# Kernel optimization log

Measured on AMD Instinct MI355X. Metric: run time of the kernel, lower is better.

## Reference

```python
import jax, jax.numpy as jnp
import numpy as np

B, S, C, V, LAT, NL = 256, 512, 256, 32, 256, 7
DILS = [1, 2, 4, 8, 16, 32, 64]
EPS = 1e-5


def setup_inputs() -> dict:
    key = jax.random.key(0)
    ks = jax.random.split(key, 24)
    s = 0.05
    inp = {
        "x": jax.random.randint(ks[0], (B, S), 0, V, dtype=jnp.int64 if jax.config.read("jax_enable_x64") else jnp.int32),
        "z": jax.random.normal(ks[1], (B, LAT), dtype=jnp.float32),
        "emb": jax.random.normal(ks[2], (V, C), dtype=jnp.float32) * s,
        "latent_W": jax.random.normal(ks[3], (LAT, C), dtype=jnp.float32) * s,
        "latent_b": jnp.zeros((C,), jnp.float32),
        "ln1_g": jnp.ones((NL, C), jnp.float32),
        "ln1_b": jnp.zeros((NL, C), jnp.float32),
        "w1": jax.random.normal(ks[4], (NL, C, C), jnp.float32) * s,
        "b1": jnp.zeros((NL, C), jnp.float32),
        "ln2_g": jnp.ones((NL, C), jnp.float32),
        "ln2_b": jnp.zeros((NL, C), jnp.float32),
        "wd": jax.random.normal(ks[5], (NL, 2, C, C), jnp.float32) * s,  # tap 0 = x[t-d], tap 1 = x[t]
        "bd": jnp.zeros((NL, C), jnp.float32),
        "ln3_g": jnp.ones((NL, C), jnp.float32),
        "ln3_b": jnp.zeros((NL, C), jnp.float32),
        "we": jax.random.normal(ks[6], (NL, C, C), jnp.float32) * s,
        "be": jnp.zeros((NL, C), jnp.float32),
        "wg": jax.random.normal(ks[7], (NL, C, C), jnp.float32) * s,
        "bg": jnp.zeros((NL, C), jnp.float32),
        "out_W": jax.random.normal(ks[8], (C, V), jnp.float32) * s,
        "out_b": jnp.zeros((V,), jnp.float32),
    }
    return inp


def _ln(h, g, b):
    mu = h.mean(-1, keepdims=True)
    var = jnp.mean((h - mu) ** 2, axis=-1, keepdims=True)
    return (h - mu) * jax.lax.rsqrt(var + EPS) * g + b


def _lrelu(h):
    return jnp.where(h >= 0, h, 0.01 * h)


def reference(x, z, emb, latent_W, latent_b, ln1_g, ln1_b, w1, b1,
              ln2_g, ln2_b, wd, bd, ln3_g, ln3_b, we, be, wg, bg,
              out_W, out_b):
    # channel-last layout [B, S, C] throughout (fuses away the torch transposes)
    h = emb[x] + (z @ latent_W + latent_b)[:, None, :]
    for i, d in enumerate(DILS):
        x_inp = h
        t = _lrelu(_ln(x_inp, ln1_g[i], ln1_b[i]))
        t = t @ w1[i] + b1[i]
        t = _lrelu(_ln(t, ln2_g[i], ln2_b[i]))
        # causal dilated conv, kernel=2: out[t] = W0*x[t-d] + W1*x[t]
        t_shift = jnp.pad(t, ((0, 0), (d, 0), (0, 0)))[:, :t.shape[1], :]
        t = t_shift @ wd[i, 0] + t @ wd[i, 1] + bd[i]
        t = _lrelu(_ln(t, ln3_g[i], ln3_b[i]))
        gated = (t @ we[i] + be[i]) * jax.nn.sigmoid(t @ wg[i] + bg[i])
        h = gated + x_inp
    logits = h @ out_W + out_b                      # [B, S, V]
    lp = jax.nn.log_softmax(logits, axis=-1)
    # gather log-prob of next token: lp[:, :-1, :] at x[:, 1:]
    return jnp.take_along_axis(lp[:, :-1, :], x[:, 1:, None], axis=2)[..., 0]
```

## Files before the change

kernel.cpp:

```cpp
#include <hip/hip_runtime.h>

typedef unsigned short u16;
typedef unsigned int   u32;
typedef __attribute__((ext_vector_type(8))) short short8;
typedef __attribute__((ext_vector_type(4))) float f32x4;

struct __align__(8) u16x4 { u16 x, y, z, w; };

#define NL 7
#define M_DIM 131072

__device__ __forceinline__ float b2f(u16 u) {
  union { float f; u32 i; } c; c.i = ((u32)u) << 16; return c.f;
}
__device__ __forceinline__ u16 f2b(float f) {
  union { float f; u32 i; } c; c.f = f;
  u32 r = c.i + 0x7FFFu + ((c.i >> 16) & 1u);
  return (u16)(r >> 16);
}
__device__ __forceinline__ void gload16(const void* g, void* l) {
  __builtin_amdgcn_global_load_lds((const __attribute__((address_space(1))) void*)g,
                                   (__attribute__((address_space(3))) void*)l, 16, 0, 0);
}


__global__ __launch_bounds__(256) void conv_w1_k(const float* __restrict__ w1, u16* __restrict__ wT) {
  int idx = blockIdx.x * 256 + threadIdx.x;
  int i = idx >> 16, rem = idx & 65535;
  int n = rem >> 8, k = rem & 255;
  wT[idx] = f2b(w1[(i << 16) + (k << 8) + n]);
}

__global__ __launch_bounds__(256) void conv_wd_k(const float* __restrict__ wd, u16* __restrict__ wT) {
  int idx = blockIdx.x * 256 + threadIdx.x;
  int i = idx / 131072, rem = idx & 131071;
  int n = rem >> 9, k2 = rem & 511;
  int tap = k2 >> 8, k = k2 & 255;
  wT[idx] = f2b(wd[(((i * 2 + tap) << 8) + k) * 256 + n]);
}

__global__ __launch_bounds__(256) void conv_weg_k(const float* __restrict__ we, const float* __restrict__ wg,
                                                  u16* __restrict__ wT) {
  int idx = blockIdx.x * 256 + threadIdx.x;
  int i = idx / 131072, rem = idx & 131071;
  int src = rem >> 16, n = (rem >> 8) & 255, k = rem & 255;
  const float* W = src ? wg : we;
  wT[idx] = f2b(W[((i << 8) + k) * 256 + n]);
}

__global__ __launch_bounds__(256) void conv_wo_k(const float* __restrict__ outW, u16* __restrict__ wTo) {
  int idx = blockIdx.x * 256 + threadIdx.x;
  int v = idx >> 8, k = idx & 255;
  wTo[idx] = f2b(outW[k * 32 + v]);
}


__global__ __launch_bounds__(256) void zlat_k(const float* __restrict__ z, const float* __restrict__ W,
                                              const float* __restrict__ bias, float* __restrict__ zlat) {
  int b = blockIdx.x, c = threadIdx.x;
  float acc = bias[c];
  for (int l = 0; l < 256; ++l) acc += z[b * 256 + l] * W[l * 256 + c];
  zlat[b * 256 + c] = acc;
}


__global__ __launch_bounds__(256) void embed_k(const int* __restrict__ x, const float* __restrict__ emb,
                                               const float* __restrict__ zlat, u16* __restrict__ h) {
  int wave = threadIdx.x >> 6, lane = threadIdx.x & 63;
  int r = blockIdx.x * 4 + wave;
  int c = lane * 4;
  int tok = x[r];
  int bi = r >> 9;
  float4 ev = *(const float4*)&emb[tok * 256 + c];
  float4 zv = *(const float4*)&zlat[bi * 256 + c];
  u16x4 hb;
  hb.x = f2b(ev.x + zv.x); hb.y = f2b(ev.y + zv.y);
  hb.z = f2b(ev.z + zv.z); hb.w = f2b(ev.w + zv.w);
  *(u16x4*)&h[(long)r * 256 + c] = hb;
}


__global__ __launch_bounds__(256, 2) void gemm1_k(
    const u16* __restrict__ h, const u16* __restrict__ WT,
    const float* __restrict__ ln1g, const float* __restrict__ ln1b,
    const float* __restrict__ bias,
    const float* __restrict__ ln2g, const float* __restrict__ ln2b,
    u16* __restrict__ V)
{
  __shared__ __align__(16) u16 lA[64 * 264];
  __shared__ __align__(16) u16 lB[256 * 32];
  __shared__ float pS[64][4], pQ[64][4];
  __shared__ float muA[64], rsA[64];
  const int tid = threadIdx.x;
  const int lane = tid & 63;
  const int wv = tid >> 6;
  const int wc = wv * 64;
  const int m0 = blockIdx.x * 64;
  const int rA = tid >> 2;
  const int cSw = ((((tid & 3) - ((tid >> 3) & 3)) & 3)) * 8;
  const int lr = lane & 15;
  const int quad = lane >> 4;
  const int lq = quad * 8;
  const int sw = ((quad + ((lr >> 1) & 3)) & 3) * 8;

  {
    const int half = lane >> 5, l5 = lane & 31;
    float4 ga = *(const float4*)&ln1g[l5 * 8];
    float4 gb = *(const float4*)&ln1g[l5 * 8 + 4];
    float4 ba = *(const float4*)&ln1b[l5 * 8];
    float4 bb = *(const float4*)&ln1b[l5 * 8 + 4];
    #pragma unroll 4
    for (int it = 0; it < 8; ++it) {
      int row = wv * 16 + it * 2 + half;
      uint4 hv = *(const uint4*)(h + (long)(m0 + row) * 256 + l5 * 8);
      float v0 = b2f((u16)(hv.x & 0xffff)), v1 = b2f((u16)(hv.x >> 16));
      float v2 = b2f((u16)(hv.y & 0xffff)), v3 = b2f((u16)(hv.y >> 16));
      float v4 = b2f((u16)(hv.z & 0xffff)), v5 = b2f((u16)(hv.z >> 16));
      float v6 = b2f((u16)(hv.w & 0xffff)), v7 = b2f((u16)(hv.w >> 16));
      float s = v0 + v1 + v2 + v3 + v4 + v5 + v6 + v7;
      float q = v0*v0 + v1*v1 + v2*v2 + v3*v3 + v4*v4 + v5*v5 + v6*v6 + v7*v7;
      #pragma unroll
      for (int o = 1; o < 32; o <<= 1) { s += __shfl_xor(s, o); q += __shfl_xor(q, o); }
      float mu = s * 0.00390625f;
      float var = q * 0.00390625f - mu * mu;
      float rs = rsqrtf(var + 1e-5f);
      float y0 = (v0 - mu) * rs * ga.x + ba.x; y0 = y0 >= 0.f ? y0 : 0.01f * y0;
      float y1 = (v1 - mu) * rs * ga.y + ba.y; y1 = y1 >= 0.f ? y1 : 0.01f * y1;
      float y2 = (v2 - mu) * rs * ga.z + ba.z; y2 = y2 >= 0.f ? y2 : 0.01f * y2;
      float y3 = (v3 - mu) * rs * ga.w + ba.w; y3 = y3 >= 0.f ? y3 : 0.01f * y3;
      float y4 = (v4 - mu) * rs * gb.x + bb.x; y4 = y4 >= 0.f ? y4 : 0.01f * y4;
      float y5 = (v5 - mu) * rs * gb.y + bb.y; y5 = y5 >= 0.f ? y5 : 0.01f * y5;
      float y6 = (v6 - mu) * rs * gb.z + bb.z; y6 = y6 >= 0.f ? y6 : 0.01f * y6;
      float y7 = (v7 - mu) * rs * gb.w + bb.w; y7 = y7 >= 0.f ? y7 : 0.01f * y7;
      uint4 ov;
      ov.x = (u32)f2b(y0) | ((u32)f2b(y1) << 16);
      ov.y = (u32)f2b(y2) | ((u32)f2b(y3) << 16);
      ov.z = (u32)f2b(y4) | ((u32)f2b(y5) << 16);
      ov.w = (u32)f2b(y6) | ((u32)f2b(y7) << 16);
      *(uint4*)&lA[row * 264 + l5 * 8] = ov;
    }
  }

  f32x4 acc[4][4];
  #pragma unroll
  for (int i = 0; i < 4; ++i)
    #pragma unroll
    for (int j = 0; j < 4; ++j) {
      acc[i][j][0] = 0.f; acc[i][j][1] = 0.f; acc[i][j][2] = 0.f; acc[i][j][3] = 0.f;
    }

  for (int kt = 0; kt < 8; ++kt) {
    const int kk = kt * 32;
    const long bofs = (long)rA * 256 + kk + cSw;
    #pragma unroll
    for (int j = 0; j < 4; ++j)
      gload16(WT + bofs + (long)(64 * j) * 256, &lB[tid * 8 + j * 2048]);
    __syncthreads();

    short8 af[4], bfr[4];
    #pragma unroll
    for (int mt = 0; mt < 4; ++mt)
      af[mt] = *(const short8*)&lA[(mt * 16 + lr) * 264 + kk + lq];
    #pragma unroll
    for (int nt = 0; nt < 4; ++nt)
      bfr[nt] = *(const short8*)&lB[(wc + nt * 16 + lr) * 32 + sw];
    #pragma unroll
    for (int mt = 0; mt < 4; ++mt)
      #pragma unroll
      for (int nt = 0; nt < 4; ++nt)
        acc[mt][nt] = __builtin_amdgcn_mfma_f32_16x16x32_bf16(af[mt], bfr[nt], acc[mt][nt], 0, 0, 0);
    __syncthreads();
  }

  float biasv[4], gv[4], bv[4];
  #pragma unroll
  for (int nt = 0; nt < 4; ++nt) {
    int n = wc + nt * 16 + lr;
    biasv[nt] = bias[n]; gv[nt] = ln2g[n]; bv[nt] = ln2b[n];
  }
  #pragma unroll
  for (int mt = 0; mt < 4; ++mt)
    #pragma unroll
    for (int r = 0; r < 4; ++r) {
      float s = 0.f, q = 0.f;
      #pragma unroll
      for (int nt = 0; nt < 4; ++nt) {
        float v = acc[mt][nt][r] + biasv[nt];
        acc[mt][nt][r] = v;
        s += v; q += v * v;
      }
      #pragma unroll
      for (int o = 1; o < 16; o <<= 1) { s += __shfl_xor(s, o); q += __shfl_xor(q, o); }
      if (lr == 0) { pS[mt * 16 + quad * 4 + r][wv] = s; pQ[mt * 16 + quad * 4 + r][wv] = q; }
    }
  __syncthreads();
  if (tid < 64) {
    float S = pS[tid][0] + pS[tid][1] + pS[tid][2] + pS[tid][3];
    float Q = pQ[tid][0] + pQ[tid][1] + pQ[tid][2] + pQ[tid][3];
    float mu = S * 0.00390625f;
    float var = Q * 0.00390625f - mu * mu;
    muA[tid] = mu; rsA[tid] = rsqrtf(var + 1e-5f);
  }
  __syncthreads();
  #pragma unroll
  for (int mt = 0; mt < 4; ++mt)
    #pragma unroll
    for (int r = 0; r < 4; ++r) {
      int row = mt * 16 + quad * 4 + r;
      float mu = muA[row], rs = rsA[row];
      #pragma unroll
      for (int nt = 0; nt < 4; ++nt) {
        float y = (acc[mt][nt][r] - mu) * rs * gv[nt] + bv[nt];
        y = y >= 0.f ? y : 0.01f * y;
        V[(long)(m0 + row) * 256 + wc + nt * 16 + lr] = f2b(y);
      }
    }
}


__global__ __launch_bounds__(256, 2) void conv_gate_k(
    const u16* __restrict__ A,
    const u16* __restrict__ WTd,
    int dil,
    const float* __restrict__ bd3, const float* __restrict__ g3, const float* __restrict__ bb3,
    const u16* __restrict__ WTe, const u16* __restrict__ WTg,
    const float* __restrict__ bev_, const float* __restrict__ bgv_,
    u16* __restrict__ h)
{
  __shared__ __align__(16) u16 pT[64 * 264];
  __shared__ __align__(16) u16 stg[16384];
  __shared__ float pS[64][4], pQ[64][4];
  __shared__ float muA[64], rsA[64];

  const int tid = threadIdx.x;
  const int lane = tid & 63;
  const int wv = tid >> 6;
  const int wc = wv * 64;
  const int m0 = blockIdx.x * 64;
  const int rA = tid >> 2;
  const int cSw = ((((tid & 3) - ((tid >> 3) & 3)) & 3)) * 8;
  const int lr = lane & 15;
  const int quad = lane >> 4;
  const int lq = quad * 8;
  const int sw = ((quad + ((lr >> 1) & 3)) & 3) * 8;
  const int mm = m0 + rA;
  const int s1 = mm & 511;
  const bool fixBlk = (m0 & 511) == 0;

  f32x4 acc[4][4];
  #pragma unroll
  for (int i = 0; i < 4; ++i)
    #pragma unroll
    for (int j = 0; j < 4; ++j) {
      acc[i][j][0] = 0.f; acc[i][j][1] = 0.f; acc[i][j][2] = 0.f; acc[i][j][3] = 0.f;
    }

#define STAGE_P1(KT) do {                                                        \
    const int kt_ = (KT);                                                        \
    const int kk_ = (kt_ & 7) * 32;                                              \
    const int r_ = (kt_ < 8 && s1 >= dil) ? (mm - dil) : mm;                     \
    gload16(A + (long)r_ * 256 + kk_ + cSw, &stg[tid * 8]);                      \
    const u16* bSrc_ = WTd + kt_ * 32 + cSw;                                     \
    gload16(bSrc_ + (long)rA * 512,         &stg[2048 + tid * 8]);               \
    gload16(bSrc_ + (long)(rA + 64) * 512,  &stg[2048 + tid * 8 + 2048]);        \
    gload16(bSrc_ + (long)(rA + 128) * 512, &stg[2048 + tid * 8 + 4096]);        \
    gload16(bSrc_ + (long)(rA + 192) * 512, &stg[2048 + tid * 8 + 6144]);        \
  } while (0)

  STAGE_P1(0);
  __syncthreads();

  for (int kt = 0; kt < 16; ++kt) {
    if (fixBlk && kt < 8) {
      if (rA < dil) { uint4 zz; zz.x = 0; zz.y = 0; zz.z = 0; zz.w = 0; *(uint4*)&stg[tid * 8] = zz; }
      __syncthreads();
    }
    short8 af[4], bfr[4];
    #pragma unroll
    for (int mt = 0; mt < 4; ++mt)
      af[mt] = *(const short8*)&stg[(mt * 16 + lr) * 32 + sw];
    #pragma unroll
    for (int nt = 0; nt < 4; ++nt)
      bfr[nt] = *(const short8*)&stg[2048 + (wc + nt * 16 + lr) * 32 + sw];
    __syncthreads();
    if (kt < 15) STAGE_P1(kt + 1);
    #pragma unroll
    for (int mt = 0; mt < 4; ++mt)
      #pragma unroll
      for (int nt = 0; nt < 4; ++nt)
        acc[mt][nt] = __builtin_amdgcn_mfma_f32_16x16x32_bf16(af[mt], bfr[nt], acc[mt][nt], 0, 0, 0);
    __syncthreads();
  }
#undef STAGE_P1

#define STAGE_P2(KT) do {                                                        \
    const long bofs_ = (long)rA * 256 + (KT) * 32 + cSw;                         \
    gload16(WTe + bofs_,              &stg[tid * 8]);                            \
    gload16(WTe + bofs_ + 64L * 256,  &stg[tid * 8 + 2048]);                     \
    gload16(WTe + bofs_ + 128L * 256, &stg[tid * 8 + 4096]);                     \
    gload16(WTe + bofs_ + 192L * 256, &stg[tid * 8 + 6144]);                     \
    gload16(WTg + bofs_,              &stg[8192 + tid * 8]);                     \
    gload16(WTg + bofs_ + 64L * 256,  &stg[8192 + tid * 8 + 2048]);              \
    gload16(WTg + bofs_ + 128L * 256, &stg[8192 + tid * 8 + 4096]);              \
    gload16(WTg + bofs_ + 192L * 256, &stg[8192 + tid * 8 + 6144]);              \
  } while (0)

  STAGE_P2(0);

  float b3v[4], g3v[4], o3v[4];
  #pragma unroll
  for (int nt = 0; nt < 4; ++nt) {
    int n = wc + nt * 16 + lr;
    b3v[nt] = bd3[n]; g3v[nt] = g3[n]; o3v[nt] = bb3[n];
  }
  #pragma unroll
  for (int mt = 0; mt < 4; ++mt)
    #pragma unroll
    for (int r = 0; r < 4; ++r) {
      float s = 0.f, q = 0.f;
      #pragma unroll
      for (int nt = 0; nt < 4; ++nt) {
        float v = acc[mt][nt][r] + b3v[nt];
        acc[mt][nt][r] = v;
        s += v; q += v * v;
      }
      #pragma unroll
      for (int o = 1; o < 16; o <<= 1) { s += __shfl_xor(s, o); q += __shfl_xor(q, o); }
      if (lr == 0) { pS[mt * 16 + quad * 4 + r][wv] = s; pQ[mt * 16 + quad * 4 + r][wv] = q; }
    }
  __syncthreads();
  if (tid < 64) {
    float S = pS[tid][0] + pS[tid][1] + pS[tid][2] + pS[tid][3];
    float Q = pQ[tid][0] + pQ[tid][1] + pQ[tid][2] + pQ[tid][3];
    float mu = S * 0.00390625f;
    float var = Q * 0.00390625f - mu * mu;
    muA[tid] = mu; rsA[tid] = rsqrtf(var + 1e-5f);
  }
  __syncthreads();
  #pragma unroll
  for (int mt = 0; mt < 4; ++mt)
    #pragma unroll
    for (int r = 0; r < 4; ++r) {
      int row = mt * 16 + quad * 4 + r;
      float mu = muA[row], rs = rsA[row];
      #pragma unroll
      for (int nt = 0; nt < 4; ++nt) {
        float y = (acc[mt][nt][r] - mu) * rs * g3v[nt] + o3v[nt];
        y = y >= 0.f ? y : 0.01f * y;
        pT[row * 264 + wc + nt * 16 + lr] = f2b(y);
      }
    }
  __syncthreads();

  f32x4 accE[4][4], accG[4][4];
  #pragma unroll
  for (int i = 0; i < 4; ++i)
    #pragma unroll
    for (int j = 0; j < 4; ++j) {
      accE[i][j][0] = 0.f; accE[i][j][1] = 0.f; accE[i][j][2] = 0.f; accE[i][j][3] = 0.f;
      accG[i][j][0] = 0.f; accG[i][j][1] = 0.f; accG[i][j][2] = 0.f; accG[i][j][3] = 0.f;
    }

  for (int kt = 0; kt < 8; ++kt) {
    const int kk = kt * 32;
    short8 paf[4], bfe[4], bfg[4];
    #pragma unroll
    for (int mt = 0; mt < 4; ++mt)
      paf[mt] = *(const short8*)&pT[(mt * 16 + lr) * 264 + kk + lq];
    #pragma unroll
    for (int nt = 0; nt < 4; ++nt) {
      bfe[nt] = *(const short8*)&stg[(wc + nt * 16 + lr) * 32 + sw];
      bfg[nt] = *(const short8*)&stg[8192 + (wc + nt * 16 + lr) * 32 + sw];
    }
    __syncthreads();
    if (kt < 7) STAGE_P2(kt + 1);
    #pragma unroll
    for (int mt = 0; mt < 4; ++mt)
      #pragma unroll
      for (int nt = 0; nt < 4; ++nt) {
        accE[mt][nt] = __builtin_amdgcn_mfma_f32_16x16x32_bf16(paf[mt], bfe[nt], accE[mt][nt], 0, 0, 0);
        accG[mt][nt] = __builtin_amdgcn_mfma_f32_16x16x32_bf16(paf[mt], bfg[nt], accG[mt][nt], 0, 0, 0);
      }
    __syncthreads();
  }
#undef STAGE_P2

  float bev[4], bgv[4];
  #pragma unroll
  for (int nt = 0; nt < 4; ++nt) {
    int n = wc + nt * 16 + lr;
    bev[nt] = bev_[n]; bgv[nt] = bgv_[n];
  }
  #pragma unroll
  for (int mt = 0; mt < 4; ++mt)
    #pragma unroll
    for (int r = 0; r < 4; ++r) {
      int row = mt * 16 + quad * 4 + r;
      long off = (long)(m0 + row) * 256;
      #pragma unroll
      for (int nt = 0; nt < 4; ++nt) {
        int n = wc + nt * 16 + lr;
        float e = accE[mt][nt][r] + bev[nt];
        float gg = accG[mt][nt][r] + bgv[nt];
        float hn = e * (1.f / (1.f + expf(-gg))) + b2f(h[off + n]);
        h[off + n] = f2b(hn);
      }
    }
}


__global__ __launch_bounds__(256) void final_k(const u16* __restrict__ h, const u16* __restrict__ WTo,
                                               const float* __restrict__ outb, const int* __restrict__ x,
                                               float* __restrict__ out) {
  __shared__ u16 lW[32 * 264];
  const int tid = threadIdx.x;
  const int lane = tid & 63;
  const int wv = tid >> 6;
  const int mBase = blockIdx.x * 256 + wv * 64;

  #pragma unroll
  for (int j = 0; j < 4; ++j) {
    int chunk = tid + 256 * j;
    int v = chunk >> 5, k8 = chunk & 31;
    uint4 w4 = *(const uint4*)(WTo + v * 256 + k8 * 8);
    *(uint4*)&lW[v * 264 + k8 * 8] = w4;
  }
  __syncthreads();

  const int lq = (lane >> 4) * 8;
  const int lr = lane & 15;
  const int quad = lane >> 4;

  f32x4 acc[4][2];
  #pragma unroll
  for (int mt = 0; mt < 4; ++mt) {
    acc[mt][0][0] = 0.f; acc[mt][0][1] = 0.f; acc[mt][0][2] = 0.f; acc[mt][0][3] = 0.f;
    acc[mt][1][0] = 0.f; acc[mt][1][1] = 0.f; acc[mt][1][2] = 0.f; acc[mt][1][3] = 0.f;
  }

  for (int kt = 0; kt < 8; ++kt) {
    short8 bf0 = *(const short8*)&lW[lr * 264 + kt * 32 + lq];
    short8 bf1 = *(const short8*)&lW[(16 + lr) * 264 + kt * 32 + lq];
    #pragma unroll
    for (int mt = 0; mt < 4; ++mt) {
      short8 af = *(const short8*)(h + (long)(mBase + mt * 16 + lr) * 256 + kt * 32 + lq);
      acc[mt][0] = __builtin_amdgcn_mfma_f32_16x16x32_bf16(af, bf0, acc[mt][0], 0, 0, 0);
      acc[mt][1] = __builtin_amdgcn_mfma_f32_16x16x32_bf16(af, bf1, acc[mt][1], 0, 0, 0);
    }
  }

  float ob0 = outb[lr], ob1 = outb[16 + lr];
  #pragma unroll
  for (int mt = 0; mt < 4; ++mt)
    #pragma unroll
    for (int r = 0; r < 4; ++r) {
      int row = mBase + mt * 16 + quad * 4 + r;
      float lo = acc[mt][0][r] + ob0;
      float hi = acc[mt][1][r] + ob1;
      float mx = fmaxf(lo, hi);
      #pragma unroll
      for (int o = 1; o < 16; o <<= 1) mx = fmaxf(mx, __shfl_xor(mx, o));
      float se = expf(lo - mx) + expf(hi - mx);
      #pragma unroll
      for (int o = 1; o < 16; o <<= 1) se += __shfl_xor(se, o);
      int s = row & 511;
      int xa = (s == 511) ? row : (row + 1);
      int tok = x[xa];
      float lg = (tok < 16) ? lo : hi;
      float lp = lg - mx - logf(se);
      if (s != 511 && lr == (tok & 15))
        out[(row >> 9) * 511 + s] = lp;
    }
}


extern "C" void kernel_launch(void* const* d_in, const int* in_sizes, int n_in,
                              void* d_out, int out_size, void* d_ws, size_t ws_size,
                              hipStream_t stream) {
  const int*   x    = (const int*)d_in[0];
  const float* z    = (const float*)d_in[1];
  const float* emb  = (const float*)d_in[2];
  const float* latW = (const float*)d_in[3];
  const float* latb = (const float*)d_in[4];
  const float* ln1g = (const float*)d_in[5];
  const float* ln1b = (const float*)d_in[6];
  const float* w1   = (const float*)d_in[7];
  const float* b1   = (const float*)d_in[8];
  const float* ln2g = (const float*)d_in[9];
  const float* ln2b = (const float*)d_in[10];
  const float* wd   = (const float*)d_in[11];
  const float* bd   = (const float*)d_in[12];
  const float* ln3g = (const float*)d_in[13];
  const float* ln3b = (const float*)d_in[14];
  const float* we   = (const float*)d_in[15];
  const float* be   = (const float*)d_in[16];
  const float* wg   = (const float*)d_in[17];
  const float* bg   = (const float*)d_in[18];
  const float* outW = (const float*)d_in[19];
  const float* outb = (const float*)d_in[20];

  char* ws = (char*)d_ws;
  u16*   h    = (u16*)(ws + 0);
  u16*   bufA = (u16*)(ws + 67108864);
  float* zlat = (float*)(ws + 201326592);
  u16*   wT1  = (u16*)(ws + 201588736);
  u16*   wTd  = (u16*)(ws + 202506240);
  u16*   wTeg = (u16*)(ws + 204341248);
  u16*   wTo  = (u16*)(ws + 206176256);

  conv_w1_k <<<1792, 256, 0, stream>>>(w1, wT1);
  conv_wd_k <<<3584, 256, 0, stream>>>(wd, wTd);
  conv_weg_k<<<3584, 256, 0, stream>>>(we, wg, wTeg);
  conv_wo_k <<<32, 256, 0, stream>>>(outW, wTo);
  zlat_k    <<<256, 256, 0, stream>>>(z, latW, latb, zlat);
  embed_k   <<<M_DIM / 4, 256, 0, stream>>>(x, emb, zlat, h);

  for (int i = 0; i < NL; ++i) {
    int d = 1 << i;
    gemm1_k<<<M_DIM / 64, 256, 0, stream>>>(
        h, wT1 + i * 65536, ln1g + i * 256, ln1b + i * 256, b1 + i * 256,
        ln2g + i * 256, ln2b + i * 256, bufA);
    conv_gate_k<<<M_DIM / 64, 256, 0, stream>>>(
        bufA, wTd + i * 131072, d,
        bd + i * 256, ln3g + i * 256, ln3b + i * 256,
        wTeg + i * 131072, wTeg + i * 131072 + 65536,
        be + i * 256, bg + i * 256, h);
  }

  final_k<<<M_DIM / 256, 256, 0, stream>>>(h, wTo, outb, x, (float*)d_out);
}
```

Measured before the change: 1.467 ms.

## Double-buffer conv_gate staging with explicit waitcnt and split E/G GEMM loops

```diff
diff --git a/kernel.cpp b/kernel.cpp
--- a/kernel.cpp
+++ b/kernel.cpp
@@ -9,6 +9,10 @@
 
 #define NL 7
 #define M_DIM 131072
+
+#define VMW(N) asm volatile("s_waitcnt vmcnt(" #N ")" ::: "memory")
+#define LGW()  asm volatile("s_waitcnt lgkmcnt(0)" ::: "memory")
+#define BAR()  __builtin_amdgcn_s_barrier()
 
 __device__ __forceinline__ float b2f(u16 u) {
   union { float f; u32 i; } c; c.i = ((u32)u) << 16; return c.f;
@@ -228,7 +232,7 @@
     u16* __restrict__ h)
 {
   __shared__ __align__(16) u16 pT[64 * 264];
-  __shared__ __align__(16) u16 stg[16384];
+  __shared__ __align__(16) u16 stg[20480];
   __shared__ float pS[64][4], pQ[64][4];
   __shared__ float muA[64], rsA[64];
 
@@ -246,6 +250,25 @@
   const int mm = m0 + rA;
   const int s1 = mm & 511;
   const bool fixBlk = (m0 & 511) == 0;
+  const short8 zero8 = {0, 0, 0, 0, 0, 0, 0, 0};
+
+  auto STAGE1 = [&](int kt, int bb) {
+    const int kkk = (kt & 7) * 32;
+    const int rr = (kt < 8 && s1 >= dil) ? (mm - dil) : mm;
+    gload16(A + (long)rr * 256 + kkk + cSw, &stg[bb + tid * 8]);
+    const u16* bS = WTd + kt * 32 + cSw;
+    gload16(bS + (long)rA * 512,          &stg[bb + 2048 + tid * 8]);
+    gload16(bS + (long)(rA + 64) * 512,   &stg[bb + 4096 + tid * 8]);
+    gload16(bS + (long)(rA + 128) * 512,  &stg[bb + 6144 + tid * 8]);
+    gload16(bS + (long)(rA + 192) * 512,  &stg[bb + 8192 + tid * 8]);
+  };
+  auto STAGE_W = [&](const u16* __restrict__ W, int kt, int bb) {
+    const long bofs = (long)rA * 256 + kt * 32 + cSw;
+    gload16(W + bofs,              &stg[bb + tid * 8]);
+    gload16(W + bofs + 64L * 256,  &stg[bb + 2048 + tid * 8]);
+    gload16(W + bofs + 128L * 256, &stg[bb + 4096 + tid * 8]);
+    gload16(W + bofs + 192L * 256, &stg[bb + 6144 + tid * 8]);
+  };
 
   f32x4 acc[4][4];
   #pragma unroll
@@ -255,57 +278,40 @@
       acc[i][j][0] = 0.f; acc[i][j][1] = 0.f; acc[i][j][2] = 0.f; acc[i][j][3] = 0.f;
     }
 
-#define STAGE_P1(KT) do {                                                        \
-    const int kt_ = (KT);                                                        \
-    const int kk_ = (kt_ & 7) * 32;                                              \
-    const int r_ = (kt_ < 8 && s1 >= dil) ? (mm - dil) : mm;                     \
-    gload16(A + (long)r_ * 256 + kk_ + cSw, &stg[tid * 8]);                      \
-    const u16* bSrc_ = WTd + kt_ * 32 + cSw;                                     \
-    gload16(bSrc_ + (long)rA * 512,         &stg[2048 + tid * 8]);               \
-    gload16(bSrc_ + (long)(rA + 64) * 512,  &stg[2048 + tid * 8 + 2048]);        \
-    gload16(bSrc_ + (long)(rA + 128) * 512, &stg[2048 + tid * 8 + 4096]);        \
-    gload16(bSrc_ + (long)(rA + 192) * 512, &stg[2048 + tid * 8 + 6144]);        \
-  } while (0)
-
-  STAGE_P1(0);
-  __syncthreads();
-
-  for (int kt = 0; kt < 16; ++kt) {
-    if (fixBlk && kt < 8) {
-      if (rA < dil) { uint4 zz; zz.x = 0; zz.y = 0; zz.z = 0; zz.w = 0; *(uint4*)&stg[tid * 8] = zz; }
-      __syncthreads();
-    }
+  STAGE1(0, 0);
+  STAGE1(1, 10240);
+  VMW(5);
+  BAR();
+
+  #pragma unroll
+  for (int r = 0; r < 16; ++r) {
+    const int bb = (r & 1) * 10240;
     short8 af[4], bfr[4];
     #pragma unroll
     for (int mt = 0; mt < 4; ++mt)
-      af[mt] = *(const short8*)&stg[(mt * 16 + lr) * 32 + sw];
+      af[mt] = *(const short8*)&stg[bb + (mt * 16 + lr) * 32 + sw];
     #pragma unroll
     for (int nt = 0; nt < 4; ++nt)
-      bfr[nt] = *(const short8*)&stg[2048 + (wc + nt * 16 + lr) * 32 + sw];
-    __syncthreads();
-    if (kt < 15) STAGE_P1(kt + 1);
+      bfr[nt] = *(const short8*)&stg[bb + 2048 + (wc + nt * 16 + lr) * 32 + sw];
+    LGW();
+    BAR();
+    if (r <= 13)      STAGE1(r + 2, bb);
+    else if (r == 14) STAGE_W(WTe, 0, 0);
+    else              STAGE_W(WTe, 1, 8192);
+    if (fixBlk && r < 8) {
+      #pragma unroll
+      for (int mt = 0; mt < 4; ++mt)
+        if (mt * 16 + lr < dil) af[mt] = zero8;
+    }
     #pragma unroll
     for (int mt = 0; mt < 4; ++mt)
       #pragma unroll
       for (int nt = 0; nt < 4; ++nt)
         acc[mt][nt] = __builtin_amdgcn_mfma_f32_16x16x32_bf16(af[mt], bfr[nt], acc[mt][nt], 0, 0, 0);
-    __syncthreads();
-  }
-#undef STAGE_P1
-
-#define STAGE_P2(KT) do {                                                        \
-    const long bofs_ = (long)rA * 256 + (KT) * 32 + cSw;                         \
-    gload16(WTe + bofs_,              &stg[tid * 8]);                            \
-    gload16(WTe + bofs_ + 64L * 256,  &stg[tid * 8 + 2048]);                     \
-    gload16(WTe + bofs_ + 128L * 256, &stg[tid * 8 + 4096]);                     \
-    gload16(WTe + bofs_ + 192L * 256, &stg[tid * 8 + 6144]);                     \
-    gload16(WTg + bofs_,              &stg[8192 + tid * 8]);                     \
-    gload16(WTg + bofs_ + 64L * 256,  &stg[8192 + tid * 8 + 2048]);              \
-    gload16(WTg + bofs_ + 128L * 256, &stg[8192 + tid * 8 + 4096]);              \
-    gload16(WTg + bofs_ + 192L * 256, &stg[8192 + tid * 8 + 6144]);              \
-  } while (0)
-
-  STAGE_P2(0);
+    if (r <= 13)      VMW(5);
+    else if (r == 14) VMW(4);
+    BAR();
+  }
 
   float b3v[4], g3v[4], o3v[4];
   #pragma unroll
@@ -328,7 +334,7 @@
       for (int o = 1; o < 16; o <<= 1) { s += __shfl_xor(s, o); q += __shfl_xor(q, o); }
       if (lr == 0) { pS[mt * 16 + quad * 4 + r][wv] = s; pQ[mt * 16 + quad * 4 + r][wv] = q; }
     }
-  __syncthreads();
+  LGW(); BAR();
   if (tid < 64) {
     float S = pS[tid][0] + pS[tid][1] + pS[tid][2] + pS[tid][3];
     float Q = pQ[tid][0] + pQ[tid][1] + pQ[tid][2] + pQ[tid][3];
@@ -336,7 +342,7 @@
     float var = Q * 0.00390625f - mu * mu;
     muA[tid] = mu; rsA[tid] = rsqrtf(var + 1e-5f);
   }
-  __syncthreads();
+  LGW(); BAR();
   #pragma unroll
   for (int mt = 0; mt < 4; ++mt)
     #pragma unroll
@@ -350,7 +356,7 @@
         pT[row * 264 + wc + nt * 16 + lr] = f2b(y);
       }
     }
-  __syncthreads();
+  LGW(); VMW(4); BAR();
 
   f32x4 accE[4][4], accG[4][4];
   #pragma unroll
@@ -361,29 +367,50 @@
       accG[i][j][0] = 0.f; accG[i][j][1] = 0.f; accG[i][j][2] = 0.f; accG[i][j][3] = 0.f;
     }
 
-  for (int kt = 0; kt < 8; ++kt) {
-    const int kk = kt * 32;
-    short8 paf[4], bfe[4], bfg[4];
-    #pragma unroll
-    for (int mt = 0; mt < 4; ++mt)
-      paf[mt] = *(const short8*)&pT[(mt * 16 + lr) * 264 + kk + lq];
-    #pragma unroll
-    for (int nt = 0; nt < 4; ++nt) {
-      bfe[nt] = *(const short8*)&stg[(wc + nt * 16 + lr) * 32 + sw];
-      bfg[nt] = *(const short8*)&stg[8192 + (wc + nt * 16 + lr) * 32 + sw];
-    }
-    __syncthreads();
-    if (kt < 7) STAGE_P2(kt + 1);
-    #pragma unroll
-    for (int mt = 0; mt < 4; ++mt)
-      #pragma unroll
-      for (int nt = 0; nt < 4; ++nt) {
+  #pragma unroll
+  for (int r = 0; r < 8; ++r) {
+    const int bb = (r & 1) * 8192;
+    short8 paf[4], bfe[4];
+    #pragma unroll
+    for (int mt = 0; mt < 4; ++mt)
+      paf[mt] = *(const short8*)&pT[(mt * 16 + lr) * 264 + r * 32 + lq];
+    #pragma unroll
+    for (int nt = 0; nt < 4; ++nt)
+      bfe[nt] = *(const short8*)&stg[bb + (wc + nt * 16 + lr) * 32 + sw];
+    LGW(); BAR();
+    if (r <= 5)      STAGE_W(WTe, r + 2, bb);
+    else if (r == 6) STAGE_W(WTg, 0, 0);
+    else             STAGE_W(WTg, 1, 8192);
+    #pragma unroll
+    for (int mt = 0; mt < 4; ++mt)
+      #pragma unroll
+      for (int nt = 0; nt < 4; ++nt)
         accE[mt][nt] = __builtin_amdgcn_mfma_f32_16x16x32_bf16(paf[mt], bfe[nt], accE[mt][nt], 0, 0, 0);
+    VMW(4);
+    BAR();
+  }
+
+  #pragma unroll
+  for (int r = 0; r < 8; ++r) {
+    const int bb = (r & 1) * 8192;
+    short8 paf[4], bfg[4];
+    #pragma unroll
+    for (int mt = 0; mt < 4; ++mt)
+      paf[mt] = *(const short8*)&pT[(mt * 16 + lr) * 264 + r * 32 + lq];
+    #pragma unroll
+    for (int nt = 0; nt < 4; ++nt)
+      bfg[nt] = *(const short8*)&stg[bb + (wc + nt * 16 + lr) * 32 + sw];
+    LGW(); BAR();
+    if (r <= 5) STAGE_W(WTg, r + 2, bb);
+    #pragma unroll
+    for (int mt = 0; mt < 4; ++mt)
+      #pragma unroll
+      for (int nt = 0; nt < 4; ++nt)
         accG[mt][nt] = __builtin_amdgcn_mfma_f32_16x16x32_bf16(paf[mt], bfg[nt], accG[mt][nt], 0, 0, 0);
-      }
-    __syncthreads();
-  }
-#undef STAGE_P2
+    if (r <= 5)      VMW(4);
+    else if (r == 6) VMW(0);
+    BAR();
+  }
 
   float bev[4], bgv[4];
   #pragma unroll
```

Result: faster. 1.436 ms (-2.1%).

## Load GEMM operands directly from global memory into registers, dropping LDS staging

Applied to the files above, without the earlier changes.

```diff
diff --git a/kernel.cpp b/kernel.cpp
--- a/kernel.cpp
+++ b/kernel.cpp
@@ -17,10 +17,6 @@
   union { float f; u32 i; } c; c.f = f;
   u32 r = c.i + 0x7FFFu + ((c.i >> 16) & 1u);
   return (u16)(r >> 16);
-}
-__device__ __forceinline__ void gload16(const void* g, void* l) {
-  __builtin_amdgcn_global_load_lds((const __attribute__((address_space(1))) void*)g,
-                                   (__attribute__((address_space(3))) void*)l, 16, 0, 0);
 }
 
 
@@ -80,7 +76,7 @@
 }
 
 
-__global__ __launch_bounds__(256, 2) void gemm1_k(
+__global__ __launch_bounds__(256, 4) void gemm1_k(
     const u16* __restrict__ h, const u16* __restrict__ WT,
     const float* __restrict__ ln1g, const float* __restrict__ ln1b,
     const float* __restrict__ bias,
@@ -88,7 +84,6 @@
     u16* __restrict__ V)
 {
   __shared__ __align__(16) u16 lA[64 * 264];
-  __shared__ __align__(16) u16 lB[256 * 32];
   __shared__ float pS[64][4], pQ[64][4];
   __shared__ float muA[64], rsA[64];
   const int tid = threadIdx.x;
@@ -96,12 +91,9 @@
   const int wv = tid >> 6;
   const int wc = wv * 64;
   const int m0 = blockIdx.x * 64;
-  const int rA = tid >> 2;
-  const int cSw = ((((tid & 3) - ((tid >> 3) & 3)) & 3)) * 8;
   const int lr = lane & 15;
   const int quad = lane >> 4;
   const int lq = quad * 8;
-  const int sw = ((quad + ((lr >> 1) & 3)) & 3) * 8;
 
   {
     const int half = lane >> 5, l5 = lane & 31;
@@ -149,27 +141,27 @@
       acc[i][j][0] = 0.f; acc[i][j][1] = 0.f; acc[i][j][2] = 0.f; acc[i][j][3] = 0.f;
     }
 
+  const u16* bp[4];
+  #pragma unroll
+  for (int nt = 0; nt < 4; ++nt) bp[nt] = WT + (long)(wc + nt * 16 + lr) * 256 + lq;
+
+  __syncthreads();
+
+  #pragma unroll
   for (int kt = 0; kt < 8; ++kt) {
     const int kk = kt * 32;
-    const long bofs = (long)rA * 256 + kk + cSw;
-    #pragma unroll
-    for (int j = 0; j < 4; ++j)
-      gload16(WT + bofs + (long)(64 * j) * 256, &lB[tid * 8 + j * 2048]);
-    __syncthreads();
-
     short8 af[4], bfr[4];
+    #pragma unroll
+    for (int nt = 0; nt < 4; ++nt)
+      bfr[nt] = *(const short8*)(bp[nt] + kk);
     #pragma unroll
     for (int mt = 0; mt < 4; ++mt)
       af[mt] = *(const short8*)&lA[(mt * 16 + lr) * 264 + kk + lq];
     #pragma unroll
-    for (int nt = 0; nt < 4; ++nt)
-      bfr[nt] = *(const short8*)&lB[(wc + nt * 16 + lr) * 32 + sw];
-    #pragma unroll
     for (int mt = 0; mt < 4; ++mt)
       #pragma unroll
       for (int nt = 0; nt < 4; ++nt)
         acc[mt][nt] = __builtin_amdgcn_mfma_f32_16x16x32_bf16(af[mt], bfr[nt], acc[mt][nt], 0, 0, 0);
-    __syncthreads();
   }
 
   float biasv[4], gv[4], bv[4];
@@ -228,7 +220,6 @@
     u16* __restrict__ h)
 {
   __shared__ __align__(16) u16 pT[64 * 264];
-  __shared__ __align__(16) u16 stg[16384];
   __shared__ float pS[64][4], pQ[64][4];
   __shared__ float muA[64], rsA[64];
 
@@ -237,15 +228,10 @@
   const int wv = tid >> 6;
   const int wc = wv * 64;
   const int m0 = blockIdx.x * 64;
-  const int rA = tid >> 2;
-  const int cSw = ((((tid & 3) - ((tid >> 3) & 3)) & 3)) * 8;
   const int lr = lane & 15;
   const int quad = lane >> 4;
   const int lq = quad * 8;
-  const int sw = ((quad + ((lr >> 1) & 3)) & 3) * 8;
-  const int mm = m0 + rA;
-  const int s1 = mm & 511;
-  const bool fixBlk = (m0 & 511) == 0;
+  const short8 zero8 = {0, 0, 0, 0, 0, 0, 0, 0};
 
   f32x4 acc[4][4];
   #pragma unroll
@@ -255,57 +241,43 @@
       acc[i][j][0] = 0.f; acc[i][j][1] = 0.f; acc[i][j][2] = 0.f; acc[i][j][3] = 0.f;
     }
 
-#define STAGE_P1(KT) do {                                                        \
-    const int kt_ = (KT);                                                        \
-    const int kk_ = (kt_ & 7) * 32;                                              \
-    const int r_ = (kt_ < 8 && s1 >= dil) ? (mm - dil) : mm;                     \
-    gload16(A + (long)r_ * 256 + kk_ + cSw, &stg[tid * 8]);                      \
-    const u16* bSrc_ = WTd + kt_ * 32 + cSw;                                     \
-    gload16(bSrc_ + (long)rA * 512,         &stg[2048 + tid * 8]);               \
-    gload16(bSrc_ + (long)(rA + 64) * 512,  &stg[2048 + tid * 8 + 2048]);        \
-    gload16(bSrc_ + (long)(rA + 128) * 512, &stg[2048 + tid * 8 + 4096]);        \
-    gload16(bSrc_ + (long)(rA + 192) * 512, &stg[2048 + tid * 8 + 6144]);        \
-  } while (0)
-
-  STAGE_P1(0);
-  __syncthreads();
-
+  const u16* a0p[4];
+  const u16* a1p[4];
+  bool zz[4];
+  #pragma unroll
+  for (int mt = 0; mt < 4; ++mt) {
+    int row = m0 + mt * 16 + lr;
+    int ss = row & 511;
+    zz[mt] = ss < dil;
+    a1p[mt] = A + (long)row * 256 + lq;
+    a0p[mt] = A + (long)(zz[mt] ? row : row - dil) * 256 + lq;
+  }
+  const u16* bdp[4];
+  #pragma unroll
+  for (int nt = 0; nt < 4; ++nt) bdp[nt] = WTd + (long)(wc + nt * 16 + lr) * 512 + lq;
+
+  #pragma unroll
   for (int kt = 0; kt < 16; ++kt) {
-    if (fixBlk && kt < 8) {
-      if (rA < dil) { uint4 zz; zz.x = 0; zz.y = 0; zz.z = 0; zz.w = 0; *(uint4*)&stg[tid * 8] = zz; }
-      __syncthreads();
-    }
+    const int kk = (kt & 7) * 32;
     short8 af[4], bfr[4];
     #pragma unroll
-    for (int mt = 0; mt < 4; ++mt)
-      af[mt] = *(const short8*)&stg[(mt * 16 + lr) * 32 + sw];
-    #pragma unroll
     for (int nt = 0; nt < 4; ++nt)
-      bfr[nt] = *(const short8*)&stg[2048 + (wc + nt * 16 + lr) * 32 + sw];
-    __syncthreads();
-    if (kt < 15) STAGE_P1(kt + 1);
+      bfr[nt] = *(const short8*)(bdp[nt] + kt * 32);
+    #pragma unroll
+    for (int mt = 0; mt < 4; ++mt) {
+      if (kt < 8) {
+        af[mt] = *(const short8*)(a0p[mt] + kk);
+        if (zz[mt]) af[mt] = zero8;
+      } else {
+        af[mt] = *(const short8*)(a1p[mt] + kk);
+      }
+    }
     #pragma unroll
     for (int mt = 0; mt < 4; ++mt)
       #pragma unroll
       for (int nt = 0; nt < 4; ++nt)
         acc[mt][nt] = __builtin_amdgcn_mfma_f32_16x16x32_bf16(af[mt], bfr[nt], acc[mt][nt], 0, 0, 0);
-    __syncthreads();
-  }
-#undef STAGE_P1
-
-#define STAGE_P2(KT) do {                                                        \
-    const long bofs_ = (long)rA * 256 + (KT) * 32 + cSw;                         \
-    gload16(WTe + bofs_,              &stg[tid * 8]);                            \
-    gload16(WTe + bofs_ + 64L * 256,  &stg[tid * 8 + 2048]);                     \
-    gload16(WTe + bofs_ + 128L * 256, &stg[tid * 8 + 4096]);                     \
-    gload16(WTe + bofs_ + 192L * 256, &stg[tid * 8 + 6144]);                     \
-    gload16(WTg + bofs_,              &stg[8192 + tid * 8]);                     \
-    gload16(WTg + bofs_ + 64L * 256,  &stg[8192 + tid * 8 + 2048]);              \
-    gload16(WTg + bofs_ + 128L * 256, &stg[8192 + tid * 8 + 4096]);              \
-    gload16(WTg + bofs_ + 192L * 256, &stg[8192 + tid * 8 + 6144]);              \
-  } while (0)
-
-  STAGE_P2(0);
+  }
 
   float b3v[4], g3v[4], o3v[4];
   #pragma unroll
@@ -361,19 +333,25 @@
       accG[i][j][0] = 0.f; accG[i][j][1] = 0.f; accG[i][j][2] = 0.f; accG[i][j][3] = 0.f;
     }
 
+  const u16* bep[4]; const u16* bgp[4];
+  #pragma unroll
+  for (int nt = 0; nt < 4; ++nt) {
+    long ro = (long)(wc + nt * 16 + lr) * 256 + lq;
+    bep[nt] = WTe + ro; bgp[nt] = WTg + ro;
+  }
+
+  #pragma unroll
   for (int kt = 0; kt < 8; ++kt) {
     const int kk = kt * 32;
     short8 paf[4], bfe[4], bfg[4];
     #pragma unroll
+    for (int nt = 0; nt < 4; ++nt) {
+      bfe[nt] = *(const short8*)(bep[nt] + kk);
+      bfg[nt] = *(const short8*)(bgp[nt] + kk);
+    }
+    #pragma unroll
     for (int mt = 0; mt < 4; ++mt)
       paf[mt] = *(const short8*)&pT[(mt * 16 + lr) * 264 + kk + lq];
-    #pragma unroll
-    for (int nt = 0; nt < 4; ++nt) {
-      bfe[nt] = *(const short8*)&stg[(wc + nt * 16 + lr) * 32 + sw];
-      bfg[nt] = *(const short8*)&stg[8192 + (wc + nt * 16 + lr) * 32 + sw];
-    }
-    __syncthreads();
-    if (kt < 7) STAGE_P2(kt + 1);
     #pragma unroll
     for (int mt = 0; mt < 4; ++mt)
       #pragma unroll
@@ -381,9 +359,7 @@
         accE[mt][nt] = __builtin_amdgcn_mfma_f32_16x16x32_bf16(paf[mt], bfe[nt], accE[mt][nt], 0, 0, 0);
         accG[mt][nt] = __builtin_amdgcn_mfma_f32_16x16x32_bf16(paf[mt], bfg[nt], accG[mt][nt], 0, 0, 0);
       }
-    __syncthreads();
-  }
-#undef STAGE_P2
+  }
 
   float bev[4], bgv[4];
   #pragma unroll
```

New measurement: 1.982 ms. 1.35x slower.

## Shrink LDS footprint to fit three blocks per CU in fused layer kernels

Applied to the files above, without the earlier changes.

```diff
diff --git a/kernel.cpp b/kernel.cpp
--- a/kernel.cpp
+++ b/kernel.cpp
@@ -21,6 +21,9 @@
 __device__ __forceinline__ void gload16(const void* g, void* l) {
   __builtin_amdgcn_global_load_lds((const __attribute__((address_space(1))) void*)g,
                                    (__attribute__((address_space(3))) void*)l, 16, 0, 0);
+}
+__device__ __forceinline__ int xIdx(int row, int chunk) {
+  return row * 256 + (((chunk) ^ (row & 7)) << 3);
 }
 
 
@@ -80,17 +83,19 @@
 }
 
 
-__global__ __launch_bounds__(256, 2) void gemm1_k(
+__global__ __launch_bounds__(256, 3) void gemm1_k(
     const u16* __restrict__ h, const u16* __restrict__ WT,
     const float* __restrict__ ln1g, const float* __restrict__ ln1b,
     const float* __restrict__ bias,
     const float* __restrict__ ln2g, const float* __restrict__ ln2b,
     u16* __restrict__ V)
 {
-  __shared__ __align__(16) u16 lA[64 * 264];
+  __shared__ __align__(16) u16 lA[64 * 256];
   __shared__ __align__(16) u16 lB[256 * 32];
-  __shared__ float pS[64][4], pQ[64][4];
-  __shared__ float muA[64], rsA[64];
+  float* pS  = (float*)lB;
+  float* pQ  = (float*)(lB + 512);
+  float* muA = (float*)(lB + 1024);
+  float* rsA = (float*)(lB + 1152);
   const int tid = threadIdx.x;
   const int lane = tid & 63;
   const int wv = tid >> 6;
@@ -100,7 +105,6 @@
   const int cSw = ((((tid & 3) - ((tid >> 3) & 3)) & 3)) * 8;
   const int lr = lane & 15;
   const int quad = lane >> 4;
-  const int lq = quad * 8;
   const int sw = ((quad + ((lr >> 1) & 3)) & 3) * 8;
 
   {
@@ -137,7 +141,7 @@
       ov.y = (u32)f2b(y2) | ((u32)f2b(y3) << 16);
       ov.z = (u32)f2b(y4) | ((u32)f2b(y5) << 16);
       ov.w = (u32)f2b(y6) | ((u32)f2b(y7) << 16);
-      *(uint4*)&lA[row * 264 + l5 * 8] = ov;
+      *(uint4*)&lA[xIdx(row, l5)] = ov;
     }
   }
 
@@ -150,8 +154,7 @@
     }
 
   for (int kt = 0; kt < 8; ++kt) {
-    const int kk = kt * 32;
-    const long bofs = (long)rA * 256 + kk + cSw;
+    const long bofs = (long)rA * 256 + kt * 32 + cSw;
     #pragma unroll
     for (int j = 0; j < 4; ++j)
       gload16(WT + bofs + (long)(64 * j) * 256, &lB[tid * 8 + j * 2048]);
@@ -160,7 +163,7 @@
     short8 af[4], bfr[4];
     #pragma unroll
     for (int mt = 0; mt < 4; ++mt)
-      af[mt] = *(const short8*)&lA[(mt * 16 + lr) * 264 + kk + lq];
+      af[mt] = *(const short8*)&lA[xIdx(mt * 16 + lr, 4 * kt + quad)];
     #pragma unroll
     for (int nt = 0; nt < 4; ++nt)
       bfr[nt] = *(const short8*)&lB[(wc + nt * 16 + lr) * 32 + sw];
@@ -191,12 +194,12 @@
       }
       #pragma unroll
       for (int o = 1; o < 16; o <<= 1) { s += __shfl_xor(s, o); q += __shfl_xor(q, o); }
-      if (lr == 0) { pS[mt * 16 + quad * 4 + r][wv] = s; pQ[mt * 16 + quad * 4 + r][wv] = q; }
+      if (lr == 0) { pS[(mt * 16 + quad * 4 + r) * 4 + wv] = s; pQ[(mt * 16 + quad * 4 + r) * 4 + wv] = q; }
     }
   __syncthreads();
   if (tid < 64) {
-    float S = pS[tid][0] + pS[tid][1] + pS[tid][2] + pS[tid][3];
-    float Q = pQ[tid][0] + pQ[tid][1] + pQ[tid][2] + pQ[tid][3];
+    float S = pS[tid * 4 + 0] + pS[tid * 4 + 1] + pS[tid * 4 + 2] + pS[tid * 4 + 3];
+    float Q = pQ[tid * 4 + 0] + pQ[tid * 4 + 1] + pQ[tid * 4 + 2] + pQ[tid * 4 + 3];
     float mu = S * 0.00390625f;
     float var = Q * 0.00390625f - mu * mu;
     muA[tid] = mu; rsA[tid] = rsqrtf(var + 1e-5f);
@@ -218,7 +221,7 @@
 }
 
 
-__global__ __launch_bounds__(256, 2) void conv_gate_k(
+__global__ __launch_bounds__(256, 3) void conv_gate_k(
     const u16* __restrict__ A,
     const u16* __restrict__ WTd,
     int dil,
@@ -227,10 +230,13 @@
     const float* __restrict__ bev_, const float* __restrict__ bgv_,
     u16* __restrict__ h)
 {
-  __shared__ __align__(16) u16 pT[64 * 264];
-  __shared__ __align__(16) u16 stg[16384];
-  __shared__ float pS[64][4], pQ[64][4];
-  __shared__ float muA[64], rsA[64];
+  __shared__ __align__(16) u16 pT[64 * 256];
+  __shared__ __align__(16) u16 stg[10240];
+  float* pS  = (float*)stg;
+  float* pQ  = (float*)(stg + 512);
+  float* muA = (float*)(stg + 1024);
+  float* rsA = (float*)(stg + 1152);
+  u16* stgW = stg + 2048;
 
   const int tid = threadIdx.x;
   const int lane = tid & 63;
@@ -241,11 +247,15 @@
   const int cSw = ((((tid & 3) - ((tid >> 3) & 3)) & 3)) * 8;
   const int lr = lane & 15;
   const int quad = lane >> 4;
-  const int lq = quad * 8;
   const int sw = ((quad + ((lr >> 1) & 3)) & 3) * 8;
   const int mm = m0 + rA;
   const int s1 = mm & 511;
-  const bool fixBlk = (m0 & 511) == 0;
+  const short8 zero8 = {0, 0, 0, 0, 0, 0, 0, 0};
+
+  bool zz[4];
+  #pragma unroll
+  for (int mt = 0; mt < 4; ++mt)
+    zz[mt] = ((m0 + mt * 16 + lr) & 511) < dil;
 
   f32x4 acc[4][4];
   #pragma unroll
@@ -255,35 +265,28 @@
       acc[i][j][0] = 0.f; acc[i][j][1] = 0.f; acc[i][j][2] = 0.f; acc[i][j][3] = 0.f;
     }
 
-#define STAGE_P1(KT) do {                                                        \
-    const int kt_ = (KT);                                                        \
-    const int kk_ = (kt_ & 7) * 32;                                              \
-    const int r_ = (kt_ < 8 && s1 >= dil) ? (mm - dil) : mm;                     \
-    gload16(A + (long)r_ * 256 + kk_ + cSw, &stg[tid * 8]);                      \
-    const u16* bSrc_ = WTd + kt_ * 32 + cSw;                                     \
-    gload16(bSrc_ + (long)rA * 512,         &stg[2048 + tid * 8]);               \
-    gload16(bSrc_ + (long)(rA + 64) * 512,  &stg[2048 + tid * 8 + 2048]);        \
-    gload16(bSrc_ + (long)(rA + 128) * 512, &stg[2048 + tid * 8 + 4096]);        \
-    gload16(bSrc_ + (long)(rA + 192) * 512, &stg[2048 + tid * 8 + 6144]);        \
-  } while (0)
-
-  STAGE_P1(0);
-  __syncthreads();
-
   for (int kt = 0; kt < 16; ++kt) {
-    if (fixBlk && kt < 8) {
-      if (rA < dil) { uint4 zz; zz.x = 0; zz.y = 0; zz.z = 0; zz.w = 0; *(uint4*)&stg[tid * 8] = zz; }
-      __syncthreads();
-    }
+    const int kk = (kt & 7) * 32;
+    {
+      const int rr = (kt < 8 && s1 >= dil) ? (mm - dil) : mm;
+      gload16(A + (long)rr * 256 + kk + cSw, &stg[tid * 8]);
+      const u16* bS = WTd + kt * 32 + cSw;
+      gload16(bS + (long)rA * 512,         &stgW[tid * 8]);
+      gload16(bS + (long)(rA + 64) * 512,  &stgW[tid * 8 + 2048]);
+      gload16(bS + (long)(rA + 128) * 512, &stgW[tid * 8 + 4096]);
+      gload16(bS + (long)(rA + 192) * 512, &stgW[tid * 8 + 6144]);
+    }
+    __syncthreads();
+
     short8 af[4], bfr[4];
     #pragma unroll
-    for (int mt = 0; mt < 4; ++mt)
+    for (int mt = 0; mt < 4; ++mt) {
       af[mt] = *(const short8*)&stg[(mt * 16 + lr) * 32 + sw];
+      if (kt < 8 && zz[mt]) af[mt] = zero8;
+    }
     #pragma unroll
     for (int nt = 0; nt < 4; ++nt)
-      bfr[nt] = *(const short8*)&stg[2048 + (wc + nt * 16 + lr) * 32 + sw];
-    __syncthreads();
-    if (kt < 15) STAGE_P1(kt + 1);
+      bfr[nt] = *(const short8*)&stgW[(wc + nt * 16 + lr) * 32 + sw];
     #pragma unroll
     for (int mt = 0; mt < 4; ++mt)
       #pragma unroll
@@ -291,21 +294,14 @@
         acc[mt][nt] = __builtin_amdgcn_mfma_f32_16x16x32_bf16(af[mt], bfr[nt], acc[mt][nt], 0, 0, 0);
     __syncthreads();
   }
-#undef STAGE_P1
-
-#define STAGE_P2(KT) do {                                                        \
-    const long bofs_ = (long)rA * 256 + (KT) * 32 + cSw;                         \
-    gload16(WTe + bofs_,              &stg[tid * 8]);                            \
-    gload16(WTe + bofs_ + 64L * 256,  &stg[tid * 8 + 2048]);                     \
-    gload16(WTe + bofs_ + 128L * 256, &stg[tid * 8 + 4096]);                     \
-    gload16(WTe + bofs_ + 192L * 256, &stg[tid * 8 + 6144]);                     \
-    gload16(WTg + bofs_,              &stg[8192 + tid * 8]);                     \
-    gload16(WTg + bofs_ + 64L * 256,  &stg[8192 + tid * 8 + 2048]);              \
-    gload16(WTg + bofs_ + 128L * 256, &stg[8192 + tid * 8 + 4096]);              \
-    gload16(WTg + bofs_ + 192L * 256, &stg[8192 + tid * 8 + 6144]);              \
-  } while (0)
-
-  STAGE_P2(0);
+
+  {
+    const long bofs = (long)rA * 256 + cSw;
+    gload16(WTe + bofs,              &stgW[tid * 8]);
+    gload16(WTe + bofs + 64L * 256,  &stgW[tid * 8 + 2048]);
+    gload16(WTe + bofs + 128L * 256, &stgW[tid * 8 + 4096]);
+    gload16(WTe + bofs + 192L * 256, &stgW[tid * 8 + 6144]);
+  }
 
   float b3v[4], g3v[4], o3v[4];
   #pragma unroll
@@ -326,12 +322,12 @@
       }
       #pragma unroll
       for (int o = 1; o < 16; o <<= 1) { s += __shfl_xor(s, o); q += __shfl_xor(q, o); }
-      if (lr == 0) { pS[mt * 16 + quad * 4 + r][wv] = s; pQ[mt * 16 + quad * 4 + r][wv] = q; }
+      if (lr == 0) { pS[(mt * 16 + quad * 4 + r) * 4 + wv] = s; pQ[(mt * 16 + quad * 4 + r) * 4 + wv] = q; }
     }
   __syncthreads();
   if (tid < 64) {
-    float S = pS[tid][0] + pS[tid][1] + pS[tid][2] + pS[tid][3];
-    float Q = pQ[tid][0] + pQ[tid][1] + pQ[tid][2] + pQ[tid][3];
+    float S = pS[tid * 4 + 0] + pS[tid * 4 + 1] + pS[tid * 4 + 2] + pS[tid * 4 + 3];
+    float Q = pQ[tid * 4 + 0] + pQ[tid * 4 + 1] + pQ[tid * 4 + 2] + pQ[tid * 4 + 3];
     float mu = S * 0.00390625f;
     float var = Q * 0.00390625f - mu * mu;
     muA[tid] = mu; rsA[tid] = rsqrtf(var + 1e-5f);
@@ -345,9 +341,10 @@
       float mu = muA[row], rs = rsA[row];
       #pragma unroll
       for (int nt = 0; nt < 4; ++nt) {
+        int col = wc + nt * 16 + lr;
         float y = (acc[mt][nt][r] - mu) * rs * g3v[nt] + o3v[nt];
         y = y >= 0.f ? y : 0.01f * y;
-        pT[row * 264 + wc + nt * 16 + lr] = f2b(y);
+        pT[xIdx(row, col >> 3) + (col & 7)] = f2b(y);
       }
     }
   __syncthreads();
@@ -362,28 +359,58 @@
     }
 
   for (int kt = 0; kt < 8; ++kt) {
-    const int kk = kt * 32;
-    short8 paf[4], bfe[4], bfg[4];
-    #pragma unroll
-    for (int mt = 0; mt < 4; ++mt)
-      paf[mt] = *(const short8*)&pT[(mt * 16 + lr) * 264 + kk + lq];
-    #pragma unroll
-    for (int nt = 0; nt < 4; ++nt) {
-      bfe[nt] = *(const short8*)&stg[(wc + nt * 16 + lr) * 32 + sw];
-      bfg[nt] = *(const short8*)&stg[8192 + (wc + nt * 16 + lr) * 32 + sw];
-    }
+    short8 paf[4], bfe[4];
+    #pragma unroll
+    for (int mt = 0; mt < 4; ++mt)
+      paf[mt] = *(const short8*)&pT[xIdx(mt * 16 + lr, 4 * kt + quad)];
+    #pragma unroll
+    for (int nt = 0; nt < 4; ++nt)
+      bfe[nt] = *(const short8*)&stgW[(wc + nt * 16 + lr) * 32 + sw];
+    #pragma unroll
+    for (int mt = 0; mt < 4; ++mt)
+      #pragma unroll
+      for (int nt = 0; nt < 4; ++nt)
+        accE[mt][nt] = __builtin_amdgcn_mfma_f32_16x16x32_bf16(paf[mt], bfe[nt], accE[mt][nt], 0, 0, 0);
     __syncthreads();
-    if (kt < 7) STAGE_P2(kt + 1);
-    #pragma unroll
-    for (int mt = 0; mt < 4; ++mt)
-      #pragma unroll
-      for (int nt = 0; nt < 4; ++nt) {
-        accE[mt][nt] = __builtin_amdgcn_mfma_f32_16x16x32_bf16(paf[mt], bfe[nt], accE[mt][nt], 0, 0, 0);
+    if (kt < 7) {
+      const long bofs = (long)rA * 256 + (kt + 1) * 32 + cSw;
+      gload16(WTe + bofs,              &stgW[tid * 8]);
+      gload16(WTe + bofs + 64L * 256,  &stgW[tid * 8 + 2048]);
+      gload16(WTe + bofs + 128L * 256, &stgW[tid * 8 + 4096]);
+      gload16(WTe + bofs + 192L * 256, &stgW[tid * 8 + 6144]);
+    } else {
+      const long bofs = (long)rA * 256 + cSw;
+      gload16(WTg + bofs,              &stgW[tid * 8]);
+      gload16(WTg + bofs + 64L * 256,  &stgW[tid * 8 + 2048]);
+      gload16(WTg + bofs + 128L * 256, &stgW[tid * 8 + 4096]);
+      gload16(WTg + bofs + 192L * 256, &stgW[tid * 8 + 6144]);
+    }
+    __syncthreads();
+  }
+
+  for (int kt = 0; kt < 8; ++kt) {
+    short8 paf[4], bfg[4];
+    #pragma unroll
+    for (int mt = 0; mt < 4; ++mt)
+      paf[mt] = *(const short8*)&pT[xIdx(mt * 16 + lr, 4 * kt + quad)];
+    #pragma unroll
+    for (int nt = 0; nt < 4; ++nt)
+      bfg[nt] = *(const short8*)&stgW[(wc + nt * 16 + lr) * 32 + sw];
+    #pragma unroll
+    for (int mt = 0; mt < 4; ++mt)
+      #pragma unroll
+      for (int nt = 0; nt < 4; ++nt)
         accG[mt][nt] = __builtin_amdgcn_mfma_f32_16x16x32_bf16(paf[mt], bfg[nt], accG[mt][nt], 0, 0, 0);
-      }
-    __syncthreads();
-  }
-#undef STAGE_P2
+    if (kt < 7) {
+      __syncthreads();
+      const long bofs = (long)rA * 256 + (kt + 1) * 32 + cSw;
+      gload16(WTg + bofs,              &stgW[tid * 8]);
+      gload16(WTg + bofs + 64L * 256,  &stgW[tid * 8 + 2048]);
+      gload16(WTg + bofs + 128L * 256, &stgW[tid * 8 + 4096]);
+      gload16(WTg + bofs + 192L * 256, &stgW[tid * 8 + 6144]);
+      __syncthreads();
+    }
+  }
 
   float bev[4], bgv[4];
   #pragma unroll
```

After: 1.468 ms. About the same (+0.1%).
